# Optimization experiments

Measured on AMD Instinct MI355X. Metric: run time of the kernel, lower is better.

The kernel has to match this reference:

```python
import jax, jax.numpy as jnp
import numpy as np

SOS = 1  # vocab.word2idx[SYM_SOS]


def _lstm_cell(x, h, c, Wih, Whh, b):
    # PyTorch LSTMCell gate order: i, f, g, o
    g = x @ Wih.T + h @ Whh.T + b
    i, f, gg, o = jnp.split(g, 4, axis=-1)
    c2 = jax.nn.sigmoid(f) * c + jax.nn.sigmoid(i) * jnp.tanh(gg)
    h2 = jax.nn.sigmoid(o) * jnp.tanh(c2)
    return h2, c2


def _attention(q, m, Wq, Wm, b, v):
    # additive attention: q [B,Dq], m [B,N,Dm] -> context [B,Dm]
    e = jnp.tanh((q @ Wq)[:, None, :] + m @ Wm + b)      # [B,N,H]
    score = jnp.einsum('bnh,h->bn', e, v)                # [B,N]
    a = jax.nn.softmax(score, axis=-1)
    return jnp.einsum('bn,bnd->bd', a, m)


def setup_inputs() -> dict:
    key = jax.random.key(0)
    ks = iter(jax.random.split(key, 32))
    B, T, V = 128, 20, 20000
    DI, DW, H = 512, 512, 1024
    s = 0.02
    d = {}
    d['img_feats'] = jax.random.normal(next(ks), (B, 36, DI), jnp.float32)
    d['ppl_feats'] = jax.random.normal(next(ks), (B, 100, DI), jnp.float32)
    d['answer_hint'] = jax.random.normal(next(ks), (B, DW), jnp.float32)
    d['question'] = jax.random.randint(next(ks), (B, T), 0, V)
    d['emb'] = jax.random.normal(next(ks), (V, DW), jnp.float32) * s
    d['pool_Wq'] = jax.random.normal(next(ks), (DW, DW), jnp.float32) * s
    d['pool_Wm'] = jax.random.normal(next(ks), (DI, DW), jnp.float32) * s
    d['pool_b'] = jnp.zeros((DW,), jnp.float32)
    d['pool_v'] = jax.random.normal(next(ks), (DW,), jnp.float32) * s
    d['img_Wq'] = jax.random.normal(next(ks), (H, H), jnp.float32) * s
    d['img_Wm'] = jax.random.normal(next(ks), (DI, H), jnp.float32) * s
    d['img_b'] = jnp.zeros((H,), jnp.float32)
    d['img_v'] = jax.random.normal(next(ks), (H,), jnp.float32) * s
    d['ppl_Wq'] = jax.random.normal(next(ks), (H, H), jnp.float32) * s
    d['ppl_Wm'] = jax.random.normal(next(ks), (DI, H), jnp.float32) * s
    d['ppl_b'] = jnp.zeros((H,), jnp.float32)
    d['ppl_v'] = jax.random.normal(next(ks), (H,), jnp.float32) * s
    d['vis_Wih'] = jax.random.normal(next(ks), (4 * H, DI + DW), jnp.float32) * s
    d['vis_Whh'] = jax.random.normal(next(ks), (4 * H, H), jnp.float32) * s
    d['vis_b'] = jnp.zeros((4 * H,), jnp.float32)
    d['lang_Wih'] = jax.random.normal(next(ks), (4 * H, H + DI), jnp.float32) * s
    d['lang_Whh'] = jax.random.normal(next(ks), (4 * H, H), jnp.float32) * s
    d['lang_b'] = jnp.zeros((4 * H,), jnp.float32)
    d['proj_W'] = jax.random.normal(next(ks), (H, V), jnp.float32) * s
    d['proj_b'] = jnp.zeros((V,), jnp.float32)
    return d


def reference(img_feats, ppl_feats, answer_hint, question, emb,
              pool_Wq, pool_Wm, pool_b, pool_v,
              img_Wq, img_Wm, img_b, img_v,
              ppl_Wq, ppl_Wm, ppl_b, ppl_v,
              vis_Wih, vis_Whh, vis_b,
              lang_Wih, lang_Whh, lang_b,
              proj_W, proj_b):
    B, T = question.shape
    H = vis_Whh.shape[1]
    # pooled image feature from answer hint (computed once)
    img_pool = _attention(answer_hint, img_feats, pool_Wq, pool_Wm, pool_b, pool_v)
    # teacher forcing inputs: SOS then question[:, :-1]
    tokens_in = jnp.concatenate(
        [jnp.full((B, 1), SOS, question.dtype), question[:, :-1]], axis=1)

    def step(carry, tok):
        h_vis, c_vis, h_lang, c_lang = carry
        dec_emb = jax.nn.relu(emb[tok])                          # [B,DW]
        x_vis = jnp.concatenate([img_pool, dec_emb], axis=-1)
        h_vis, c_vis = _lstm_cell(x_vis, h_vis, c_vis, vis_Wih, vis_Whh, vis_b)
        image_attn = _attention(h_vis, img_feats, img_Wq, img_Wm, img_b, img_v)
        ppl_attn = _attention(h_vis, ppl_feats, ppl_Wq, ppl_Wm, ppl_b, ppl_v)
        x_lang = jnp.concatenate([image_attn + ppl_attn, h_vis], axis=-1)
        h_lang, c_lang = _lstm_cell(x_lang, h_lang, c_lang, lang_Wih, lang_Whh, lang_b)
        logp = jax.nn.log_softmax(h_lang @ proj_W + proj_b, axis=-1)
        return (h_vis, c_vis, h_lang, c_lang), (logp, jnp.argmax(logp, axis=-1))

    z = jnp.zeros((B, H), img_feats.dtype)
    _, (logps, toks) = jax.lax.scan(step, (z, z, z, z), tokens_in.T)
    return jnp.transpose(logps, (1, 0, 2)), toks.T


if __name__ == '__main__':
    out = reference(**setup_inputs())
    print(out[0].shape, out[1].shape)
```

## Files before the change

kernel.cpp:

```cpp
#include <hip/hip_runtime.h>
#include <cstddef>
#include <cstdint>

using u16 = unsigned short;
typedef float    f32x4 __attribute__((ext_vector_type(4)));
typedef _Float16 f16x8 __attribute__((ext_vector_type(8)));
typedef u16      us8   __attribute__((ext_vector_type(8)));

constexpr int B  = 128;
constexpr int T  = 20;
constexpr int V  = 20000;
constexpr int DW = 512;
constexpr int H  = 1024;
constexpr int G4 = 4096;
constexpr int NI = 36;
constexpr int NP = 100;
constexpr int SOS = 1;

__device__ __forceinline__ float sigf(float x) { return 1.0f / (1.0f + expf(-x)); }
__device__ __forceinline__ u16 f16bits(_Float16 h) { u16 u; __builtin_memcpy(&u, &h, 2); return u; }

template<bool WSIDE>
__device__ __forceinline__ void split1(float x, u16& b0, u16& b1, u16& b2) {
    _Float16 h  = (_Float16)x;
    float    hf = (float)h;
    _Float16 lo = (_Float16)((x - hf) * 64.0f);
    _Float16 hs = (_Float16)(hf * (1.0f / 64.0f));
    b0 = f16bits(h);
    if constexpr (WSIDE) { b1 = f16bits(hs); b2 = f16bits(lo); }
    else                 { b1 = f16bits(lo); b2 = f16bits(hs); }
}

template<int BM, int BN, bool HAS_ADD, bool HAS_BIAS, int NSW = 0>
__global__ __launch_bounds__(256)
void gemm3(const u16* __restrict__ A, const u16* __restrict__ Bt,
           const float* __restrict__ Add, const float* __restrict__ bias,
           float* __restrict__ C, int N, int K3)
{
    __shared__ __align__(16) u16 As[BM * 64];
    __shared__ __align__(16) u16 Bs[BN * 64];
    constexpr int FR = BM / 32, FC = BN / 32, PA = BM / 32, PB = BN / 32;
    const int tid  = threadIdx.x;
    int bx = blockIdx.x, by = blockIdx.y;
    if constexpr (NSW > 0) {
        const int nt = (int)gridDim.x, mt = (int)gridDim.y;
        const int lin = by * nt + bx;
        const int sc0 = (lin / (NSW * mt)) * NSW;
        const int w   = (NSW < nt - sc0) ? NSW : (nt - sc0);
        const int r   = lin - sc0 * mt;
        bx = sc0 + r % w;
        by = r / w;
    }
    const int bm   = by * BM, bn = bx * BN;
    const int lane = tid & 63, wid = tid >> 6;
    const int wm   = (wid >> 1) * (BM / 2), wn = (wid & 1) * (BN / 2);
    const int srow = tid >> 3;
    const int scol = (tid & 7) * 8;

    f32x4 acc[FR][FC] = {};
    us8 ra[PA], rb[PB];

    auto ldg = [&](int k0) {
#pragma unroll
        for (int p = 0; p < PA; ++p)
            ra[p] = *(const us8*)(A + (size_t)(bm + p * 32 + srow) * K3 + k0 + scol);
#pragma unroll
        for (int p = 0; p < PB; ++p) {
            int n = bn + p * 32 + srow; if (n > N - 1) n = N - 1;
            rb[p] = *(const us8*)(Bt + (size_t)n * K3 + k0 + scol);
        }
    };
    ldg(0);

    for (int k0 = 0; k0 < K3; k0 += 64) {
        __syncthreads();
#pragma unroll
        for (int p = 0; p < PA; ++p) {
            const int row = p * 32 + srow;
            *(us8*)((char*)As + row * 128 + ((scol * 2) ^ ((row & 7) << 4))) = ra[p];
        }
#pragma unroll
        for (int p = 0; p < PB; ++p) {
            const int row = p * 32 + srow;
            *(us8*)((char*)Bs + row * 128 + ((scol * 2) ^ ((row & 7) << 4))) = rb[p];
        }
        __syncthreads();
        if (k0 + 64 < K3) ldg(k0 + 64);
#pragma unroll
        for (int ks = 0; ks < 2; ++ks) {
            f16x8 af[FR], bf[FC];
#pragma unroll
            for (int m = 0; m < FR; ++m) {
                const int row = wm + m * 16 + (lane & 15);
                const int cb  = (ks * 64 + ((lane >> 4) << 4)) ^ ((row & 7) << 4);
                af[m] = *(const f16x8*)((const char*)As + row * 128 + cb);
            }
#pragma unroll
            for (int n = 0; n < FC; ++n) {
                const int row = wn + n * 16 + (lane & 15);
                const int cb  = (ks * 64 + ((lane >> 4) << 4)) ^ ((row & 7) << 4);
                bf[n] = *(const f16x8*)((const char*)Bs + row * 128 + cb);
            }
#pragma unroll
            for (int m = 0; m < FR; ++m)
#pragma unroll
                for (int n = 0; n < FC; ++n)
                    acc[m][n] = __builtin_amdgcn_mfma_f32_16x16x32_f16(af[m], bf[n], acc[m][n], 0, 0, 0);
        }
    }
#pragma unroll
    for (int m = 0; m < FR; ++m) {
        const int r0 = bm + wm + m * 16 + ((lane >> 4) << 2);
#pragma unroll
        for (int n = 0; n < FC; ++n) {
            const int c = bn + wn + n * 16 + (lane & 15);
            if (c < N) {
#pragma unroll
                for (int j = 0; j < 4; ++j) {
                    float v = acc[m][n][j];
                    if constexpr (HAS_ADD)  v += Add[(size_t)(r0 + j) * N + c];
                    if constexpr (HAS_BIAS) v += bias[c];
                    C[(size_t)(r0 + j) * N + c] = v;
                }
            }
        }
    }
}

template<int EPI>
__device__ __forceinline__ void gemm_core(
    u16* __restrict__ As, u16* __restrict__ Bs,
    const u16* __restrict__ A, const u16* __restrict__ Bt,
    const float* __restrict__ Add, const float* __restrict__ bias,
    float* __restrict__ CS, u16* __restrict__ o1, u16* __restrict__ o2,
    int N, int K3, int t, int bx, int by)
{
    constexpr int BK = 192;
    const int tid  = threadIdx.x;
    const int bn   = bx * 64, bm = by * 64;
    const int lane = tid & 63, wv = tid >> 6;
    const int srow = tid >> 2;
    const int sc   = (tid & 3) * 48;
    const int swz  = (srow & 7) << 4;
    const u16* Ap = A  + (size_t)(bm + srow) * K3 + sc;
    const u16* Bp = Bt + (size_t)(bn + srow) * K3 + sc;
    char* Awp = (char*)As + srow * (BK * 2);
    char* Bwp = (char*)Bs + srow * (BK * 2);
    const int arow = wv * 16 + (lane & 15);
    const char* Arp = (const char*)As + arow * (BK * 2);
    const int aswz = (arow & 7) << 4;
    const int jl   = lane & 15;

    f32x4 acc[4] = {};
    us8 ra[6], rb[6];
#pragma unroll
    for (int i = 0; i < 6; ++i) { ra[i] = *(const us8*)(Ap + 8 * i); rb[i] = *(const us8*)(Bp + 8 * i); }

    for (int k0 = 0; k0 < K3; k0 += BK) {
        __syncthreads();
#pragma unroll
        for (int i = 0; i < 6; ++i) {
            *(us8*)(Awp + ((sc * 2 + 16 * i) ^ swz)) = ra[i];
            *(us8*)(Bwp + ((sc * 2 + 16 * i) ^ swz)) = rb[i];
        }
        __syncthreads();
        if (k0 + BK < K3) {
#pragma unroll
            for (int i = 0; i < 6; ++i) {
                ra[i] = *(const us8*)(Ap + k0 + BK + 8 * i);
                rb[i] = *(const us8*)(Bp + k0 + BK + 8 * i);
            }
        }
#pragma unroll
        for (int ks = 0; ks < BK / 32; ++ks) {
            const int cb = ks * 64 + ((lane >> 4) << 4);
            const f16x8 af = *(const f16x8*)(Arp + (cb ^ aswz));
#pragma unroll
            for (int g = 0; g < 4; ++g) {
                const int brow = g * 16 + jl;
                const f16x8 bf = *(const f16x8*)((const char*)Bs + brow * (BK * 2) + (cb ^ ((brow & 7) << 4)));
                acc[g] = __builtin_amdgcn_mfma_f32_16x16x32_f16(af, bf, acc[g], 0, 0, 0);
            }
        }
    }
    const int rb0 = bm + wv * 16 + ((lane >> 4) << 2);
    if constexpr (EPI == 0) {
#pragma unroll
        for (int g = 0; g < 4; ++g) {
            const int c = bn + g * 16 + jl;
#pragma unroll
            for (int jj = 0; jj < 4; ++jj)
                CS[(size_t)(rb0 + jj) * N + c] = acc[g][jj];
        }
    } else {
        const int j = bx * 16 + jl;
#pragma unroll
        for (int jj = 0; jj < 4; ++jj) {
            const int b = rb0 + jj;
            float gi = acc[0][jj], gf = acc[1][jj], gg = acc[2][jj], go = acc[3][jj];
            if constexpr (EPI == 1) {
                const float* ap = Add + (size_t)b * 4096 + bn + jl;
                gi += ap[0]; gf += ap[16]; gg += ap[32]; go += ap[48];
            } else {
                const float* bp = bias + bn + jl;
                gi += bp[0]; gf += bp[16]; gg += bp[32]; go += bp[48];
            }
            const float c = sigf(gf) * CS[b * 1024 + j] + sigf(gi) * tanhf(gg);
            const float h = sigf(go) * tanhf(c);
            CS[b * 1024 + j] = c;
            u16 b0, b1, b2; split1<false>(h, b0, b1, b2);
            if constexpr (EPI == 1) {
                u16* a = o1 + (size_t)b * 3072 + j;
                a[0] = b0; a[1024] = b1; a[2048] = b2;
                u16* x = o2 + (size_t)b * 7680 + 512 + j;
                x[0] = b0; x[2560] = b1; x[5120] = b2;
            } else {
                u16* x = o1 + (size_t)b * 7680 + 1536 + j;
                x[0] = b0; x[2560] = b1; x[5120] = b2;
                u16* hh = o2 + ((size_t)b * T + t) * 3072 + j;
                hh[0] = b0; hh[1024] = b1; hh[2048] = b2;
            }
        }
    }
}

__global__ __launch_bounds__(256)
void gemm_q(const u16* __restrict__ A, const u16* __restrict__ Bt,
            float* __restrict__ CS, int N, int K3)
{
    __shared__ __align__(16) u16 As[64 * 192];
    __shared__ __align__(16) u16 Bs[64 * 192];
    gemm_core<0>(As, Bs, A, Bt, nullptr, nullptr, CS, nullptr, nullptr,
                 N, K3, 0, blockIdx.x, blockIdx.y);
}

__global__ __launch_bounds__(256)
void step_combo(const u16* __restrict__ lang_A, const u16* __restrict__ langW3,
                const float* __restrict__ lang_bi, float* __restrict__ c_lang,
                u16* __restrict__ lang_o1, u16* __restrict__ h3_all,
                const u16* __restrict__ vis_A, const u16* __restrict__ visWhh3,
                const float* __restrict__ g_pre_t, float* __restrict__ c_vis,
                u16* __restrict__ vis_o1, u16* __restrict__ vis_o2, int t)
{
    __shared__ __align__(16) u16 As[64 * 192];
    __shared__ __align__(16) u16 Bs[64 * 192];
    if (blockIdx.z == 0) {
        if (t >= 1)
            gemm_core<2>(As, Bs, lang_A, langW3, nullptr, lang_bi,
                         c_lang, lang_o1, h3_all, G4, 7680, t - 1,
                         blockIdx.x, blockIdx.y);
    } else {
        if (t < T)
            gemm_core<1>(As, Bs, vis_A, visWhh3, g_pre_t, nullptr,
                         c_vis, vis_o1, vis_o2, G4, 3072, t,
                         blockIdx.x, blockIdx.y);
    }
}

template<bool WSIDE>
__global__ __launch_bounds__(256)
void split3_rows(const float* __restrict__ src, int ld, int K8,
                 u16* __restrict__ out, int Kt, int coloff)
{
    const int idx = blockIdx.x * 256 + threadIdx.x;
    const int r = idx / K8, kk = (idx - r * K8) * 8;
    const float* s = src + (size_t)r * ld + kk;
    const float4 x0 = *(const float4*)s, x1 = *(const float4*)(s + 4);
    float xs[8] = {x0.x, x0.y, x0.z, x0.w, x1.x, x1.y, x1.z, x1.w};
    us8 h, m, l;
#pragma unroll
    for (int j = 0; j < 8; ++j) { u16 a, b, c; split1<WSIDE>(xs[j], a, b, c); h[j]=a; m[j]=b; l[j]=c; }
    u16* o = out + (size_t)r * (3 * Kt) + coloff + kk;
    *(us8*)o = h; *(us8*)(o + Kt) = m; *(us8*)(o + 2 * Kt) = l;
}

__global__ __launch_bounds__(256)
void split3_lstm(const float* __restrict__ src, int ld, int K8,
                 u16* __restrict__ out, int Kt, int coloff)
{
    const int idx = blockIdx.x * 256 + threadIdx.x;
    const int r = idx / K8, kk = (idx - r * K8) * 8;
    const int g = r >> 10, j = r & 1023;
    const int orow = ((j >> 4) << 6) + (g << 4) + (j & 15);
    const float* s = src + (size_t)r * ld + kk;
    const float4 x0 = *(const float4*)s, x1 = *(const float4*)(s + 4);
    float xs[8] = {x0.x, x0.y, x0.z, x0.w, x1.x, x1.y, x1.z, x1.w};
    us8 h, m, l;
#pragma unroll
    for (int jj = 0; jj < 8; ++jj) { u16 a, b, c; split1<true>(xs[jj], a, b, c); h[jj]=a; m[jj]=b; l[jj]=c; }
    u16* o = out + (size_t)orow * (3 * Kt) + coloff + kk;
    *(us8*)o = h; *(us8*)(o + Kt) = m; *(us8*)(o + 2 * Kt) = l;
}

__global__ __launch_bounds__(256)
void permute_bias_lstm(const float* __restrict__ b, float* __restrict__ out)
{
    const int c = blockIdx.x * 256 + threadIdx.x;
    const int jg = c >> 6, g = (c >> 4) & 3, jlo = c & 15;
    out[c] = b[g * 1024 + jg * 16 + jlo];
}

__global__ __launch_bounds__(256)
void transpose_split3_w(const float* __restrict__ W, int N, int K,
                        u16* __restrict__ out)
{
    const int n0 = blockIdx.x * 64, k0 = blockIdx.y * 64;
    const int tid = threadIdx.x;
    __shared__ float ts[64][65];
    for (int i = 0; i < 16; ++i) {
        const int idx = i * 256 + tid;
        const int kl = idx >> 6, nl = idx & 63;
        float v = 0.f;
        if (n0 + nl < N) v = W[(size_t)(k0 + kl) * N + n0 + nl];
        ts[nl][kl] = v;
    }
    __syncthreads();
    for (int i = 0; i < 2; ++i) {
        const int idx = i * 256 + tid;
        const int nl = idx >> 3, kc = (idx & 7) * 8;
        if (n0 + nl < N) {
            us8 h, m, l;
#pragma unroll
            for (int j = 0; j < 8; ++j) {
                u16 a, b, c; split1<true>(ts[nl][kc + j], a, b, c);
                h[j] = a; m[j] = b; l[j] = c;
            }
            u16* o = out + (size_t)(n0 + nl) * (3 * K) + k0 + kc;
            *(us8*)o = h; *(us8*)(o + K) = m; *(us8*)(o + 2 * K) = l;
        }
    }
}

__global__ __launch_bounds__(256)
void embed_relu3(const int* __restrict__ question, const float* __restrict__ emb,
                 u16* __restrict__ demb3)
{
    const int idx = blockIdx.x * 256 + threadIdx.x;
    const int r = idx >> 6, kk = (idx & 63) * 8;
    const int t = r / B, b = r - t * B;
    const int tok = (t == 0) ? SOS : question[b * T + t - 1];
    const float* s = emb + (size_t)tok * DW + kk;
    const float4 x0 = *(const float4*)s, x1 = *(const float4*)(s + 4);
    float xs[8] = {x0.x, x0.y, x0.z, x0.w, x1.x, x1.y, x1.z, x1.w};
    us8 h, m, l;
#pragma unroll
    for (int j = 0; j < 8; ++j) {
        u16 a, b2, c; split1<false>(fmaxf(xs[j], 0.f), a, b2, c);
        h[j] = a; m[j] = b2; l[j] = c;
    }
    u16* o = demb3 + (size_t)r * 1536 + kk;
    *(us8*)o = h; *(us8*)(o + 512) = m; *(us8*)(o + 1024) = l;
}

__global__ __launch_bounds__(256)
void attn_score(const float* __restrict__ q, int qld,
                const float* __restrict__ mW, const float* __restrict__ v,
                float* __restrict__ score, int Nn, int Hd)
{
    const int n = blockIdx.x, b = blockIdx.y;
    const float* qp = q + (size_t)b * qld;
    const float* mp = mW + ((size_t)b * Nn + n) * Hd;
    float s = 0.f;
    for (int h = threadIdx.x; h < Hd; h += 256)
        s += tanhf(qp[h] + mp[h]) * v[h];
    __shared__ float red[4];
    const int lane = threadIdx.x & 63, wv = threadIdx.x >> 6;
    for (int o = 32; o; o >>= 1) s += __shfl_down(s, o, 64);
    if (lane == 0) red[wv] = s;
    __syncthreads();
    if (threadIdx.x == 0) score[(size_t)b * Nn + n] = red[0] + red[1] + red[2] + red[3];
}

__global__ __launch_bounds__(256)
void attn_ctx_pool(const float* __restrict__ score, const float* __restrict__ m,
                   u16* __restrict__ out3, int Nn)
{
    constexpr int D = 512;
    const int b = blockIdx.x;
    __shared__ float aw[128];
    __shared__ float red[8];
    const int tid = threadIdx.x, lane = tid & 63, wv = tid >> 6;
    float mx = -3.4e38f;
    for (int n = tid; n < Nn; n += 256) mx = fmaxf(mx, score[(size_t)b * Nn + n]);
    for (int o = 32; o; o >>= 1) mx = fmaxf(mx, __shfl_down(mx, o, 64));
    if (lane == 0) red[wv] = mx;
    __syncthreads();
    mx = fmaxf(fmaxf(red[0], red[1]), fmaxf(red[2], red[3]));
    float se = 0.f;
    for (int n = tid; n < Nn; n += 256) {
        float e = expf(score[(size_t)b * Nn + n] - mx);
        aw[n] = e; se += e;
    }
    for (int o = 32; o; o >>= 1) se += __shfl_down(se, o, 64);
    if (lane == 0) red[4 + wv] = se;
    __syncthreads();
    const float inv = 1.0f / (red[4] + red[5] + red[6] + red[7]);
    for (int d = tid; d < D; d += 256) {
        float s = 0.f;
        for (int n = 0; n < Nn; ++n) s += aw[n] * m[((size_t)b * Nn + n) * D + d];
        s *= inv;
        u16 b0, b1, b2; split1<false>(s, b0, b1, b2);
        u16* o = out3 + (size_t)b * 1536 + d;
        o[0] = b0; o[512] = b1; o[1024] = b2;
    }
}

__global__ __launch_bounds__(512)
void attn_fused(const float* __restrict__ qbuf,
                const float* __restrict__ img_mW, const float* __restrict__ ppl_mW,
                const float* __restrict__ img_v, const float* __restrict__ ppl_v,
                const float* __restrict__ img_feats, const float* __restrict__ ppl_feats,
                u16* __restrict__ x3)
{
    const int b = blockIdx.x;
    const int tid = threadIdx.x, lane = tid & 63, wv = tid >> 6;
    __shared__ float qs[2048];
    __shared__ float vs[2048];
    __shared__ float aw[136];
    __shared__ float awn[136];

    for (int i = tid; i < 2048; i += 512) {
        qs[i] = qbuf[(size_t)b * 2048 + i];
        vs[i] = (i < 1024) ? img_v[i] : ppl_v[i - 1024];
    }
    __syncthreads();

    for (int n = wv; n < NI; n += 8) {
        const float* mp = img_mW + ((size_t)b * NI + n) * 1024;
        float s = 0.f;
#pragma unroll
        for (int u = 0; u < 4; ++u) {
            const int h = (lane + 64 * u) * 4;
            const float4 m4 = *(const float4*)(mp + h);
            s += tanhf(qs[h+0] + m4.x) * vs[h+0] + tanhf(qs[h+1] + m4.y) * vs[h+1]
               + tanhf(qs[h+2] + m4.z) * vs[h+2] + tanhf(qs[h+3] + m4.w) * vs[h+3];
        }
        for (int o = 1; o < 64; o <<= 1) s += __shfl_xor(s, o, 64);
        if (lane == 0) aw[n] = s;
    }
    for (int n = wv; n < NP; n += 8) {
        const float* mp = ppl_mW + ((size_t)b * NP + n) * 1024;
        float s = 0.f;
#pragma unroll
        for (int u = 0; u < 4; ++u) {
            const int h = (lane + 64 * u) * 4;
            const float4 m4 = *(const float4*)(mp + h);
            s += tanhf(qs[1024+h+0] + m4.x) * vs[1024+h+0] + tanhf(qs[1024+h+1] + m4.y) * vs[1024+h+1]
               + tanhf(qs[1024+h+2] + m4.z) * vs[1024+h+2] + tanhf(qs[1024+h+3] + m4.w) * vs[1024+h+3];
        }
        for (int o = 1; o < 64; o <<= 1) s += __shfl_xor(s, o, 64);
        if (lane == 0) aw[36 + n] = s;
    }
    __syncthreads();

    if (wv == 0) {
        const float x = (lane < NI) ? aw[lane] : -3.4e38f;
        float mx = x;
        for (int o = 1; o < 64; o <<= 1) mx = fmaxf(mx, __shfl_xor(mx, o, 64));
        const float e = (lane < NI) ? expf(x - mx) : 0.f;
        float ss = e;
        for (int o = 1; o < 64; o <<= 1) ss += __shfl_xor(ss, o, 64);
        if (lane < NI) awn[lane] = e / ss;
    } else if (wv == 1) {
        const float x0 = aw[36 + lane];
        const float x1 = (lane < NP - 64) ? aw[100 + lane] : -3.4e38f;
        float mx = fmaxf(x0, x1);
        for (int o = 1; o < 64; o <<= 1) mx = fmaxf(mx, __shfl_xor(mx, o, 64));
        const float e0 = expf(x0 - mx);
        const float e1 = (lane < NP - 64) ? expf(x1 - mx) : 0.f;
        float ss = e0 + e1;
        for (int o = 1; o < 64; o <<= 1) ss += __shfl_xor(ss, o, 64);
        awn[36 + lane] = e0 / ss;
        if (lane < NP - 64) awn[100 + lane] = e1 / ss;
    }
    __syncthreads();

    {
        const int d = tid;
        float s = 0.f;
        const float* ip = img_feats + (size_t)b * NI * 512 + d;
#pragma unroll 4
        for (int n = 0; n < NI; ++n) s += awn[n] * ip[n * 512];
        const float* pp = ppl_feats + (size_t)b * NP * 512 + d;
#pragma unroll 4
        for (int n = 0; n < NP; ++n) s += awn[36 + n] * pp[n * 512];
        u16 b0, b1, b2; split1<false>(s, b0, b1, b2);
        u16* o = x3 + (size_t)b * 7680 + d;
        o[0] = b0; o[2560] = b1; o[5120] = b2;
    }
}

__global__ __launch_bounds__(256)
void add_bcast(float* __restrict__ g_pre, const float* __restrict__ g_const)
{
    const int idx = blockIdx.x * 256 + threadIdx.x;
    const int bg = idx % (B * G4 / 4);
    float4 a = ((float4*)g_pre)[idx];
    const float4 c = ((const float4*)g_const)[bg];
    a.x += c.x; a.y += c.y; a.z += c.z; a.w += c.w;
    ((float4*)g_pre)[idx] = a;
}

__global__ __launch_bounds__(256)
void zero_f(float* __restrict__ p) { p[blockIdx.x * 256 + threadIdx.x] = 0.f; }

__global__ __launch_bounds__(256)
void zero_u32(unsigned int* __restrict__ p) { p[blockIdx.x * 256 + threadIdx.x] = 0u; }

__global__ __launch_bounds__(256)
void logsm_argmax(float* __restrict__ out)
{
    const int r = blockIdx.x;
    float* row = out + (size_t)r * V;
    const int tid = threadIdx.x, lane = tid & 63, wv = tid >> 6;
    float m = -3.4e38f, s = 0.f; int mi = 0;
    for (int i4 = tid; i4 < V / 4; i4 += 256) {
        const float4 x4 = ((const float4*)row)[i4];
        const float xs[4] = {x4.x, x4.y, x4.z, x4.w};
#pragma unroll
        for (int j = 0; j < 4; ++j) {
            const float x = xs[j];
            if (x > m) { s = s * expf(m - x) + 1.f; m = x; mi = i4 * 4 + j; }
            else       s += expf(x - m);
        }
    }
    for (int o = 1; o < 64; o <<= 1) {
        const float m2 = __shfl_xor(m, o, 64);
        const float s2 = __shfl_xor(s, o, 64);
        const int  mi2 = __shfl_xor(mi, o, 64);
        if (m2 > m || (m2 == m && mi2 < mi)) { s = s2 + s * expf(m - m2); m = m2; mi = mi2; }
        else s += s2 * expf(m2 - m);
    }
    __shared__ float sm[4], ssm[4]; __shared__ int smi[4];
    __shared__ float lse_sh; __shared__ int mi_sh;
    if (lane == 0) { sm[wv] = m; ssm[wv] = s; smi[wv] = mi; }
    __syncthreads();
    if (tid == 0) {
        float M = sm[0], S = ssm[0]; int MI = smi[0];
        for (int w = 1; w < 4; ++w) {
            if (sm[w] > M || (sm[w] == M && smi[w] < MI)) { S = ssm[w] + S * expf(M - sm[w]); M = sm[w]; MI = smi[w]; }
            else S += ssm[w] * expf(sm[w] - M);
        }
        lse_sh = M + logf(S); mi_sh = MI;
    }
    __syncthreads();
    const float lse = lse_sh;
    for (int i4 = tid; i4 < V / 4; i4 += 256) {
        float4 x4 = ((const float4*)row)[i4];
        x4.x -= lse; x4.y -= lse; x4.z -= lse; x4.w -= lse;
        ((float4*)row)[i4] = x4;
    }
    if (tid == 0) out[(size_t)B * T * V + r] = (float)mi_sh;
}

extern "C" void kernel_launch(void* const* d_in, const int* in_sizes, int n_in,
                              void* d_out, int out_size, void* d_ws, size_t ws_size,
                              hipStream_t stream)
{
    (void)in_sizes; (void)n_in; (void)out_size; (void)ws_size;

    const float* img_feats   = (const float*)d_in[0];
    const float* ppl_feats   = (const float*)d_in[1];
    const float* answer_hint = (const float*)d_in[2];
    const int*   question    = (const int*)d_in[3];
    const float* emb         = (const float*)d_in[4];
    const float* pool_Wq     = (const float*)d_in[5];
    const float* pool_Wm     = (const float*)d_in[6];
    const float* pool_b      = (const float*)d_in[7];
    const float* pool_v      = (const float*)d_in[8];
    const float* img_Wq      = (const float*)d_in[9];
    const float* img_Wm      = (const float*)d_in[10];
    const float* img_b       = (const float*)d_in[11];
    const float* img_v       = (const float*)d_in[12];
    const float* ppl_Wq      = (const float*)d_in[13];
    const float* ppl_Wm      = (const float*)d_in[14];
    const float* ppl_b       = (const float*)d_in[15];
    const float* ppl_v       = (const float*)d_in[16];
    const float* vis_Wih     = (const float*)d_in[17];
    const float* vis_Whh     = (const float*)d_in[18];
    const float* vis_b       = (const float*)d_in[19];
    const float* lang_Wih    = (const float*)d_in[20];
    const float* lang_Whh    = (const float*)d_in[21];
    const float* lang_b      = (const float*)d_in[22];
    const float* proj_W      = (const float*)d_in[23];
    const float* proj_b      = (const float*)d_in[24];

    float* out = (float*)d_out;
    float* ws  = (float*)d_ws;

    size_t off = 0;
    auto alloc = [&](size_t nf) { size_t r = off; off += (nf + 63) & ~(size_t)63; return r; };
    const size_t regionX = off;
    float* g_pre   = ws + alloc((size_t)T * B * G4);
    float* pool_mW = ws + alloc((size_t)B * NI * DW);
    float* img_mW  = ws + alloc((size_t)B * NI * H);
    float* ppl_mW  = ws + alloc((size_t)B * NP * H);
    u16*   demb3   = (u16*)(ws + alloc((size_t)T * B * 1536 / 2));
    u16* img3      = (u16*)(ws + alloc((size_t)B * NI * 1536 / 2));
    u16* ppl3      = (u16*)(ws + alloc((size_t)B * NP * 1536 / 2));
    u16* hint3     = (u16*)(ws + alloc((size_t)B * 1536 / 2));
    u16* imgpool3  = (u16*)(ws + alloc((size_t)B * 1536 / 2));
    u16* visdemb3  = (u16*)(ws + alloc((size_t)G4 * 1536 / 2));
    u16* vispool3  = (u16*)(ws + alloc((size_t)G4 * 1536 / 2));
    u16* visWhh3   = (u16*)(ws + alloc((size_t)G4 * 3072 / 2));
    u16* langW3    = (u16*)(ws + alloc((size_t)G4 * 7680 / 2));
    u16* wq3t      = (u16*)(ws + alloc((size_t)2048 * 3072 / 2));
    u16* poolWq3t  = (u16*)(ws + alloc((size_t)512 * 1536 / 2));
    u16* poolWm3t  = (u16*)(ws + alloc((size_t)512 * 1536 / 2));
    u16* imgWm3t   = (u16*)(ws + alloc((size_t)1024 * 1536 / 2));
    u16* pplWm3t   = (u16*)(ws + alloc((size_t)1024 * 1536 / 2));
    float* c_vis   = ws + alloc((size_t)B * H);
    float* c_lang  = ws + alloc((size_t)B * H);
    u16* a3        = (u16*)(ws + alloc((size_t)2 * B * 3072 / 2));
    u16* x3        = (u16*)(ws + alloc((size_t)2 * B * 7680 / 2));
    u16* h3_all    = (u16*)(ws + alloc((size_t)B * T * 3072 / 2));
    float* qbuf    = ws + alloc((size_t)B * 2048);
    float* g_const = ws + alloc((size_t)B * G4);
    float* vis_bi  = ws + alloc((size_t)G4);
    float* lang_bi = ws + alloc((size_t)G4);
    float* pool_qW = ws + alloc((size_t)B * DW);
    float* pool_sc = ws + alloc((size_t)B * NI);
    u16* projW3t   = (u16*)(ws + regionX);

    const dim3 blk(256);

    zero_f<<<dim3((2 * B * H) / 256), blk, 0, stream>>>(c_vis);
    zero_u32<<<dim3((2 * B * 3072 + 2 * B * 7680) / 2 / 256), blk, 0, stream>>>((unsigned int*)a3);

    embed_relu3<<<dim3(T * B * 64 / 256), blk, 0, stream>>>(question, emb, demb3);
    permute_bias_lstm<<<dim3(16), blk, 0, stream>>>(vis_b, vis_bi);
    permute_bias_lstm<<<dim3(16), blk, 0, stream>>>(lang_b, lang_bi);
    split3_lstm<<<dim3(G4 * 64 / 256), blk, 0, stream>>>(vis_Wih + 512, 1024, 64, visdemb3, 512, 0);
    split3_lstm<<<dim3(G4 * 64 / 256), blk, 0, stream>>>(vis_Wih, 1024, 64, vispool3, 512, 0);
    split3_lstm<<<dim3(G4 * 128 / 256), blk, 0, stream>>>(vis_Whh, 1024, 128, visWhh3, 1024, 0);
    split3_lstm<<<dim3(G4 * 192 / 256), blk, 0, stream>>>(lang_Wih, 1536, 192, langW3, 2560, 0);
    split3_lstm<<<dim3(G4 * 128 / 256), blk, 0, stream>>>(lang_Whh, 1024, 128, langW3, 2560, 1536);
    split3_rows<false><<<dim3(B * NI * 64 / 256), blk, 0, stream>>>(img_feats, 512, 64, img3, 512, 0);
    split3_rows<false><<<dim3(B * NP * 64 / 256), blk, 0, stream>>>(ppl_feats, 512, 64, ppl3, 512, 0);
    split3_rows<false><<<dim3(B * 64 / 256), blk, 0, stream>>>(answer_hint, 512, 64, hint3, 512, 0);
    transpose_split3_w<<<dim3(8, 8), blk, 0, stream>>>(pool_Wq, 512, 512, poolWq3t);
    transpose_split3_w<<<dim3(8, 8), blk, 0, stream>>>(pool_Wm, 512, 512, poolWm3t);
    transpose_split3_w<<<dim3(16, 8), blk, 0, stream>>>(img_Wm, 1024, 512, imgWm3t);
    transpose_split3_w<<<dim3(16, 8), blk, 0, stream>>>(ppl_Wm, 1024, 512, pplWm3t);
    transpose_split3_w<<<dim3(16, 16), blk, 0, stream>>>(img_Wq, 1024, 1024, wq3t);
    transpose_split3_w<<<dim3(16, 16), blk, 0, stream>>>(ppl_Wq, 1024, 1024, wq3t + (size_t)1024 * 3072);

    gemm3<128, 128, false, true><<<dim3(32, 20), blk, 0, stream>>>(demb3, visdemb3, nullptr, vis_bi, g_pre, G4, 1536);
    gemm3<64, 64, false, false><<<dim3(8, 2), blk, 0, stream>>>(hint3, poolWq3t, nullptr, nullptr, pool_qW, 512, 1536);
    gemm3<128, 128, false, true><<<dim3(4, 36), blk, 0, stream>>>(img3, poolWm3t, nullptr, pool_b, pool_mW, 512, 1536);
    attn_score<<<dim3(NI, B), blk, 0, stream>>>(pool_qW, 512, pool_mW, pool_v, pool_sc, NI, 512);
    attn_ctx_pool<<<dim3(B), blk, 0, stream>>>(pool_sc, img_feats, imgpool3, NI);
    gemm3<64, 64, false, false><<<dim3(64, 2), blk, 0, stream>>>(imgpool3, vispool3, nullptr, nullptr, g_const, G4, 1536);
    add_bcast<<<dim3(T * B * G4 / 4 / 256), blk, 0, stream>>>(g_pre, g_const);
    gemm3<128, 128, false, true><<<dim3(8, 36), blk, 0, stream>>>(img3, imgWm3t, nullptr, img_b, img_mW, H, 1536);
    gemm3<128, 128, false, true><<<dim3(8, 100), blk, 0, stream>>>(ppl3, pplWm3t, nullptr, ppl_b, ppl_mW, H, 1536);

    for (int t = 0; t <= T; ++t) {
        u16* lang_A  = x3 + (size_t)((t + 1) & 1) * B * 7680;
        u16* lang_o1 = x3 + (size_t)(t & 1) * B * 7680;
        u16* vis_A   = a3 + (size_t)(t & 1) * B * 3072;
        u16* vis_o1  = a3 + (size_t)((t + 1) & 1) * B * 3072;
        u16* vis_o2  = x3 + (size_t)(t & 1) * B * 7680;
        const float* gp = g_pre + (size_t)(t < T ? t : 0) * B * G4;
        step_combo<<<dim3(64, 2, 2), blk, 0, stream>>>(
            lang_A, langW3, lang_bi, c_lang, lang_o1, h3_all,
            vis_A, visWhh3, gp, c_vis, vis_o1, vis_o2, t);
        if (t < T) {
            gemm_q<<<dim3(32, 2), blk, 0, stream>>>(vis_o1, wq3t, qbuf, 2048, 3072);
            attn_fused<<<dim3(B), dim3(512), 0, stream>>>(qbuf, img_mW, ppl_mW, img_v, ppl_v,
                                                          img_feats, ppl_feats, vis_o2);
        }
    }

    transpose_split3_w<<<dim3(313, 16), blk, 0, stream>>>(proj_W, V, 1024, projW3t);
    gemm3<128, 128, false, true, 20><<<dim3(157, 20), blk, 0, stream>>>(
        h3_all, projW3t, nullptr, proj_b, out, V, 3072);
    logsm_argmax<<<dim3(B * T), blk, 0, stream>>>(out);
}
```

Before: 3.854 ms.

## Store attention memory projections in fp16 and retile per-step GEMMs

The img/ppl memory projections (m@Wm+b) are now written as fp16 instead of fp32, halving the bytes attn_fused reads each timestep. gemm_core is templated on BN and BK: the recurrent step GEMMs use BK=384, and gemm_q uses BN=32 with twice as many blocks. The aim is less per-step memory traffic, fewer k-loop syncs, and more parallelism for the small q GEMM. In exchange, shared memory per block grows and the memory-projection values lose precision through fp16 rounding.

```diff
diff --git a/kernel.cpp b/kernel.cpp
--- a/kernel.cpp
+++ b/kernel.cpp
@@ -19,6 +19,7 @@
 
 __device__ __forceinline__ float sigf(float x) { return 1.0f / (1.0f + expf(-x)); }
 __device__ __forceinline__ u16 f16bits(_Float16 h) { u16 u; __builtin_memcpy(&u, &h, 2); return u; }
+__device__ __forceinline__ float h2f(u16 u) { _Float16 h; __builtin_memcpy(&h, &u, 2); return (float)h; }
 
 template<bool WSIDE>
 __device__ __forceinline__ void split1(float x, u16& b0, u16& b1, u16& b2) {
@@ -31,11 +32,11 @@
     else                 { b1 = f16bits(lo); b2 = f16bits(hs); }
 }
 
-template<int BM, int BN, bool HAS_ADD, bool HAS_BIAS, int NSW = 0>
+template<int BM, int BN, bool HAS_ADD, bool HAS_BIAS, int NSW = 0, bool OUTF16 = false>
 __global__ __launch_bounds__(256)
 void gemm3(const u16* __restrict__ A, const u16* __restrict__ Bt,
            const float* __restrict__ Add, const float* __restrict__ bias,
-           float* __restrict__ C, int N, int K3)
+           void* __restrict__ Cv, int N, int K3)
 {
     __shared__ __align__(16) u16 As[BM * 64];
     __shared__ __align__(16) u16 Bs[BN * 64];
@@ -120,14 +121,17 @@
                     float v = acc[m][n][j];
                     if constexpr (HAS_ADD)  v += Add[(size_t)(r0 + j) * N + c];
                     if constexpr (HAS_BIAS) v += bias[c];
-                    C[(size_t)(r0 + j) * N + c] = v;
+                    if constexpr (OUTF16)
+                        ((u16*)Cv)[(size_t)(r0 + j) * N + c] = f16bits((_Float16)v);
+                    else
+                        ((float*)Cv)[(size_t)(r0 + j) * N + c] = v;
                 }
             }
         }
     }
 }
 
-template<int EPI>
+template<int EPI, int BN, int BK>
 __device__ __forceinline__ void gemm_core(
     u16* __restrict__ As, u16* __restrict__ Bs,
     const u16* __restrict__ A, const u16* __restrict__ Bt,
@@ -135,48 +139,56 @@
     float* __restrict__ CS, u16* __restrict__ o1, u16* __restrict__ o2,
     int N, int K3, int t, int bx, int by)
 {
-    constexpr int BK = 192;
+    constexpr int NA8  = BK / 32;
+    constexpr int TPRB = 256 / BN;
+    constexpr int NB8  = (BK / TPRB) / 8;
+    constexpr int NFC  = BN / 16;
     const int tid  = threadIdx.x;
-    const int bn   = bx * 64, bm = by * 64;
+    const int bn   = bx * BN, bm = by * 64;
     const int lane = tid & 63, wv = tid >> 6;
-    const int srow = tid >> 2;
-    const int sc   = (tid & 3) * 48;
-    const int swz  = (srow & 7) << 4;
-    const u16* Ap = A  + (size_t)(bm + srow) * K3 + sc;
-    const u16* Bp = Bt + (size_t)(bn + srow) * K3 + sc;
-    char* Awp = (char*)As + srow * (BK * 2);
-    char* Bwp = (char*)Bs + srow * (BK * 2);
+    const int rowA = tid >> 2;
+    const int scA  = (tid & 3) * (BK / 4);
+    const int rowB = tid / TPRB;
+    const int scB  = (tid % TPRB) * (BK / TPRB);
+    const int swzA = (rowA & 7) << 4;
+    const int swzB = (rowB & 7) << 4;
+    const u16* Ap = A  + (size_t)(bm + rowA) * K3 + scA;
+    const u16* Bp = Bt + (size_t)(bn + rowB) * K3 + scB;
+    char* Awp = (char*)As + rowA * (BK * 2);
+    char* Bwp = (char*)Bs + rowB * (BK * 2);
     const int arow = wv * 16 + (lane & 15);
     const char* Arp = (const char*)As + arow * (BK * 2);
     const int aswz = (arow & 7) << 4;
     const int jl   = lane & 15;
 
-    f32x4 acc[4] = {};
-    us8 ra[6], rb[6];
-#pragma unroll
-    for (int i = 0; i < 6; ++i) { ra[i] = *(const us8*)(Ap + 8 * i); rb[i] = *(const us8*)(Bp + 8 * i); }
+    f32x4 acc[NFC] = {};
+    us8 ra[NA8], rb[NB8];
+#pragma unroll
+    for (int i = 0; i < NA8; ++i) ra[i] = *(const us8*)(Ap + 8 * i);
+#pragma unroll
+    for (int i = 0; i < NB8; ++i) rb[i] = *(const us8*)(Bp + 8 * i);
 
     for (int k0 = 0; k0 < K3; k0 += BK) {
         __syncthreads();
 #pragma unroll
-        for (int i = 0; i < 6; ++i) {
-            *(us8*)(Awp + ((sc * 2 + 16 * i) ^ swz)) = ra[i];
-            *(us8*)(Bwp + ((sc * 2 + 16 * i) ^ swz)) = rb[i];
-        }
+        for (int i = 0; i < NA8; ++i)
+            *(us8*)(Awp + ((scA * 2 + 16 * i) ^ swzA)) = ra[i];
+#pragma unroll
+        for (int i = 0; i < NB8; ++i)
+            *(us8*)(Bwp + ((scB * 2 + 16 * i) ^ swzB)) = rb[i];
         __syncthreads();
         if (k0 + BK < K3) {
 #pragma unroll
-            for (int i = 0; i < 6; ++i) {
-                ra[i] = *(const us8*)(Ap + k0 + BK + 8 * i);
-                rb[i] = *(const us8*)(Bp + k0 + BK + 8 * i);
-            }
+            for (int i = 0; i < NA8; ++i) ra[i] = *(const us8*)(Ap + k0 + BK + 8 * i);
+#pragma unroll
+            for (int i = 0; i < NB8; ++i) rb[i] = *(const us8*)(Bp + k0 + BK + 8 * i);
         }
 #pragma unroll
         for (int ks = 0; ks < BK / 32; ++ks) {
             const int cb = ks * 64 + ((lane >> 4) << 4);
             const f16x8 af = *(const f16x8*)(Arp + (cb ^ aswz));
 #pragma unroll
-            for (int g = 0; g < 4; ++g) {
+            for (int g = 0; g < NFC; ++g) {
                 const int brow = g * 16 + jl;
                 const f16x8 bf = *(const f16x8*)((const char*)Bs + brow * (BK * 2) + (cb ^ ((brow & 7) << 4)));
                 acc[g] = __builtin_amdgcn_mfma_f32_16x16x32_f16(af, bf, acc[g], 0, 0, 0);
@@ -186,7 +198,7 @@
     const int rb0 = bm + wv * 16 + ((lane >> 4) << 2);
     if constexpr (EPI == 0) {
 #pragma unroll
-        for (int g = 0; g < 4; ++g) {
+        for (int g = 0; g < NFC; ++g) {
             const int c = bn + g * 16 + jl;
 #pragma unroll
             for (int jj = 0; jj < 4; ++jj)
@@ -228,10 +240,10 @@
 void gemm_q(const u16* __restrict__ A, const u16* __restrict__ Bt,
             float* __restrict__ CS, int N, int K3)
 {
-    __shared__ __align__(16) u16 As[64 * 192];
-    __shared__ __align__(16) u16 Bs[64 * 192];
-    gemm_core<0>(As, Bs, A, Bt, nullptr, nullptr, CS, nullptr, nullptr,
-                 N, K3, 0, blockIdx.x, blockIdx.y);
+    __shared__ __align__(16) u16 As[64 * 384];
+    __shared__ __align__(16) u16 Bs[32 * 384];
+    gemm_core<0, 32, 384>(As, Bs, A, Bt, nullptr, nullptr, CS, nullptr, nullptr,
+                          N, K3, 0, blockIdx.x, blockIdx.y);
 }
 
 __global__ __launch_bounds__(256)
@@ -242,18 +254,18 @@
                 const float* __restrict__ g_pre_t, float* __restrict__ c_vis,
                 u16* __restrict__ vis_o1, u16* __restrict__ vis_o2, int t)
 {
-    __shared__ __align__(16) u16 As[64 * 192];
-    __shared__ __align__(16) u16 Bs[64 * 192];
+    __shared__ __align__(16) u16 As[64 * 384];
+    __shared__ __align__(16) u16 Bs[64 * 384];
     if (blockIdx.z == 0) {
         if (t >= 1)
-            gemm_core<2>(As, Bs, lang_A, langW3, nullptr, lang_bi,
-                         c_lang, lang_o1, h3_all, G4, 7680, t - 1,
-                         blockIdx.x, blockIdx.y);
+            gemm_core<2, 64, 384>(As, Bs, lang_A, langW3, nullptr, lang_bi,
+                                  c_lang, lang_o1, h3_all, G4, 7680, t - 1,
+                                  blockIdx.x, blockIdx.y);
     } else {
         if (t < T)
-            gemm_core<1>(As, Bs, vis_A, visWhh3, g_pre_t, nullptr,
-                         c_vis, vis_o1, vis_o2, G4, 3072, t,
-                         blockIdx.x, blockIdx.y);
+            gemm_core<1, 64, 384>(As, Bs, vis_A, visWhh3, g_pre_t, nullptr,
+                                  c_vis, vis_o1, vis_o2, G4, 3072, t,
+                                  blockIdx.x, blockIdx.y);
     }
 }
 
@@ -407,7 +419,7 @@
 
 __global__ __launch_bounds__(512)
 void attn_fused(const float* __restrict__ qbuf,
-                const float* __restrict__ img_mW, const float* __restrict__ ppl_mW,
+                const u16* __restrict__ img_mW, const u16* __restrict__ ppl_mW,
                 const float* __restrict__ img_v, const float* __restrict__ ppl_v,
                 const float* __restrict__ img_feats, const float* __restrict__ ppl_feats,
                 u16* __restrict__ x3)
@@ -426,27 +438,29 @@
     __syncthreads();
 
     for (int n = wv; n < NI; n += 8) {
-        const float* mp = img_mW + ((size_t)b * NI + n) * 1024;
+        const u16* mp = img_mW + ((size_t)b * NI + n) * 1024;
         float s = 0.f;
 #pragma unroll
-        for (int u = 0; u < 4; ++u) {
-            const int h = (lane + 64 * u) * 4;
-            const float4 m4 = *(const float4*)(mp + h);
-            s += tanhf(qs[h+0] + m4.x) * vs[h+0] + tanhf(qs[h+1] + m4.y) * vs[h+1]
-               + tanhf(qs[h+2] + m4.z) * vs[h+2] + tanhf(qs[h+3] + m4.w) * vs[h+3];
+        for (int u = 0; u < 2; ++u) {
+            const int h = (lane + 64 * u) * 8;
+            const us8 m8 = *(const us8*)(mp + h);
+#pragma unroll
+            for (int j = 0; j < 8; ++j)
+                s += tanhf(qs[h + j] + h2f(m8[j])) * vs[h + j];
         }
         for (int o = 1; o < 64; o <<= 1) s += __shfl_xor(s, o, 64);
         if (lane == 0) aw[n] = s;
     }
     for (int n = wv; n < NP; n += 8) {
-        const float* mp = ppl_mW + ((size_t)b * NP + n) * 1024;
+        const u16* mp = ppl_mW + ((size_t)b * NP + n) * 1024;
         float s = 0.f;
 #pragma unroll
-        for (int u = 0; u < 4; ++u) {
-            const int h = (lane + 64 * u) * 4;
-            const float4 m4 = *(const float4*)(mp + h);
-            s += tanhf(qs[1024+h+0] + m4.x) * vs[1024+h+0] + tanhf(qs[1024+h+1] + m4.y) * vs[1024+h+1]
-               + tanhf(qs[1024+h+2] + m4.z) * vs[1024+h+2] + tanhf(qs[1024+h+3] + m4.w) * vs[1024+h+3];
+        for (int u = 0; u < 2; ++u) {
+            const int h = (lane + 64 * u) * 8;
+            const us8 m8 = *(const us8*)(mp + h);
+#pragma unroll
+            for (int j = 0; j < 8; ++j)
+                s += tanhf(qs[1024 + h + j] + h2f(m8[j])) * vs[1024 + h + j];
         }
         for (int o = 1; o < 64; o <<= 1) s += __shfl_xor(s, o, 64);
         if (lane == 0) aw[36 + n] = s;
@@ -593,20 +607,20 @@
     const size_t regionX = off;
     float* g_pre   = ws + alloc((size_t)T * B * G4);
     float* pool_mW = ws + alloc((size_t)B * NI * DW);
-    float* img_mW  = ws + alloc((size_t)B * NI * H);
-    float* ppl_mW  = ws + alloc((size_t)B * NP * H);
     u16*   demb3   = (u16*)(ws + alloc((size_t)T * B * 1536 / 2));
+    u16*   hint3   = (u16*)(ws + alloc((size_t)B * 1536 / 2));
+    u16*   poolWq3t= (u16*)(ws + alloc((size_t)512 * 1536 / 2));
+    u16*   poolWm3t= (u16*)(ws + alloc((size_t)512 * 1536 / 2));
+    u16*   visdemb3= (u16*)(ws + alloc((size_t)G4 * 1536 / 2));
+    u16*   vispool3= (u16*)(ws + alloc((size_t)G4 * 1536 / 2));
+    u16* img_mW    = (u16*)(ws + alloc((size_t)B * NI * H / 2));
+    u16* ppl_mW    = (u16*)(ws + alloc((size_t)B * NP * H / 2));
     u16* img3      = (u16*)(ws + alloc((size_t)B * NI * 1536 / 2));
     u16* ppl3      = (u16*)(ws + alloc((size_t)B * NP * 1536 / 2));
-    u16* hint3     = (u16*)(ws + alloc((size_t)B * 1536 / 2));
     u16* imgpool3  = (u16*)(ws + alloc((size_t)B * 1536 / 2));
-    u16* visdemb3  = (u16*)(ws + alloc((size_t)G4 * 1536 / 2));
-    u16* vispool3  = (u16*)(ws + alloc((size_t)G4 * 1536 / 2));
     u16* visWhh3   = (u16*)(ws + alloc((size_t)G4 * 3072 / 2));
     u16* langW3    = (u16*)(ws + alloc((size_t)G4 * 7680 / 2));
     u16* wq3t      = (u16*)(ws + alloc((size_t)2048 * 3072 / 2));
-    u16* poolWq3t  = (u16*)(ws + alloc((size_t)512 * 1536 / 2));
-    u16* poolWm3t  = (u16*)(ws + alloc((size_t)512 * 1536 / 2));
     u16* imgWm3t   = (u16*)(ws + alloc((size_t)1024 * 1536 / 2));
     u16* pplWm3t   = (u16*)(ws + alloc((size_t)1024 * 1536 / 2));
     float* c_vis   = ws + alloc((size_t)B * H);
@@ -652,8 +666,8 @@
     attn_ctx_pool<<<dim3(B), blk, 0, stream>>>(pool_sc, img_feats, imgpool3, NI);
     gemm3<64, 64, false, false><<<dim3(64, 2), blk, 0, stream>>>(imgpool3, vispool3, nullptr, nullptr, g_const, G4, 1536);
     add_bcast<<<dim3(T * B * G4 / 4 / 256), blk, 0, stream>>>(g_pre, g_const);
-    gemm3<128, 128, false, true><<<dim3(8, 36), blk, 0, stream>>>(img3, imgWm3t, nullptr, img_b, img_mW, H, 1536);
-    gemm3<128, 128, false, true><<<dim3(8, 100), blk, 0, stream>>>(ppl3, pplWm3t, nullptr, ppl_b, ppl_mW, H, 1536);
+    gemm3<128, 128, false, true, 0, true><<<dim3(8, 36), blk, 0, stream>>>(img3, imgWm3t, nullptr, img_b, img_mW, H, 1536);
+    gemm3<128, 128, false, true, 0, true><<<dim3(8, 100), blk, 0, stream>>>(ppl3, pplWm3t, nullptr, ppl_b, ppl_mW, H, 1536);
 
     for (int t = 0; t <= T; ++t) {
         u16* lang_A  = x3 + (size_t)((t + 1) & 1) * B * 7680;
@@ -666,7 +680,7 @@
             lang_A, langW3, lang_bi, c_lang, lang_o1, h3_all,
             vis_A, visWhh3, gp, c_vis, vis_o1, vis_o2, t);
         if (t < T) {
-            gemm_q<<<dim3(32, 2), blk, 0, stream>>>(vis_o1, wq3t, qbuf, 2048, 3072);
+            gemm_q<<<dim3(64, 2), blk, 0, stream>>>(vis_o1, wq3t, qbuf, 2048, 3072);
             attn_fused<<<dim3(B), dim3(512), 0, stream>>>(qbuf, img_mW, ppl_mW, img_v, ppl_v,
                                                           img_feats, ppl_feats, vis_o2);
         }
```

Result: faster. 3.658 ms (-5.1%).
